# Optimization experiments

Measured on AMD Instinct MI355X. Metric: run time of the kernel, lower is better.

## Reference

```python
import jax, jax.numpy as jnp
import numpy as np

D = 512
H = 8
DH = D // H


def setup_inputs() -> dict:
    key = jax.random.key(0)
    ks = jax.random.split(key, 6)
    B, S = 2, 4096
    scale = 1.0 / np.sqrt(D)
    x = jax.random.normal(ks[0], (B, S, D), dtype=jnp.float32)
    W_q = jax.random.normal(ks[1], (D, D), dtype=jnp.float32) * scale
    W_k = jax.random.normal(ks[2], (D, D), dtype=jnp.float32) * scale
    W_v = jax.random.normal(ks[3], (D, D), dtype=jnp.float32) * scale
    W_proj = jax.random.normal(ks[4], (D, D), dtype=jnp.float32) * scale
    b_proj = jax.random.normal(ks[5], (D,), dtype=jnp.float32) * 0.01
    return {"x": x, "W_q": W_q, "W_k": W_k, "W_v": W_v,
            "W_proj": W_proj, "b_proj": b_proj}


def reference(x, W_q, W_k, W_v, W_proj, b_proj):
    B, S, _ = x.shape
    # torch Linear: y = x @ W.T
    def proj(W):
        y = jnp.einsum('bsd,ed->bse', x, W)
        return y.reshape(B, S, H, DH).transpose(0, 2, 1, 3)  # [B,H,S,DH]
    q, k, v = proj(W_q), proj(W_k), proj(W_v)
    scores = jnp.einsum('bhqd,bhkd->bhqk', q, k) / np.sqrt(DH)  # [B,H,S,S]
    causal = jnp.tril(jnp.ones((S, S), dtype=bool))
    neg = jnp.finfo(scores.dtype).min
    scores = jnp.where(causal[None, None, :, :], scores, neg)
    w = jax.nn.softmax(scores, axis=-1)
    attn = jnp.einsum('bhqk,bhkd->bhqd', w, v)  # [B,H,S,DH]
    attn = attn.transpose(0, 2, 1, 3).reshape(B, S, D)
    return jnp.einsum('bsd,ed->bse', attn, W_proj) + b_proj
```

## Files before the change

kernel.cpp:

```cpp
#include <hip/hip_runtime.h>
#include <hip/hip_bf16.h>
#include <stdint.h>

#define D_MODEL 512
#define NH 8
#define DH 64
#define SEQ 4096
#define NBH 16

typedef __attribute__((ext_vector_type(8))) short bf16x8;
typedef __attribute__((ext_vector_type(4))) float f32x4;
typedef __attribute__((ext_vector_type(16))) float f32x16;

#define CSCALE 0.18033688011112042f

__device__ __forceinline__ uint32_t pkbf(float a, float b) {
    union { float f; uint32_t u; } x, y; x.f = a; y.f = b;
    return __builtin_amdgcn_perm(y.u + 0x8000u, x.u + 0x8000u, 0x07060302u);
}

#define SWZ(R) (((R) + ((R) >> 2)) & 3)

__device__ __forceinline__ bf16x8 cvt8(float4 u, float4 v, float s) {
    union { uint32_t w[4]; bf16x8 h; } r;
    r.w[0] = pkbf(u.x * s, u.y * s); r.w[1] = pkbf(u.z * s, u.w * s);
    r.w[2] = pkbf(v.x * s, v.y * s); r.w[3] = pkbf(v.z * s, v.w * s);
    return r.h;
}

__global__ __launch_bounds__(256) void qkv_kernel(
    const float* __restrict__ x,
    const float* __restrict__ Wq, const float* __restrict__ Wk,
    const float* __restrict__ Wv,
    short* __restrict__ Qb, short* __restrict__ Kb, short* __restrict__ Vt)
{
    __shared__ __align__(16) short at[2][4096];
    __shared__ __align__(16) short bt[2][4096];

    const int tid  = threadIdx.x;
    const int wave = tid >> 6;
    const int lane = tid & 63;
    const int ln = lane & 15, quad = lane >> 4;
    const int z = blockIdx.z;
    const float* W = (z == 0) ? Wq : (z == 1) ? Wk : Wv;
    const float wscale = (z == 0) ? CSCALE : 1.0f;
    const int m0 = blockIdx.x * 128;
    const int n0 = blockIdx.y * 128;
    const int mh = (wave & 1) * 64, nh = (wave >> 1) * 64;

    const int ck0 = tid, ck1 = tid + 256;
    const int R0 = ck0 >> 2, R1 = ck1 >> 2;
    const int c0 = (ck0 & 3) ^ SWZ(R0), c1 = (ck1 & 3) ^ SWZ(R1);

    float4 ra[4], rb[4];
    auto loadAB = [&](int kc) {
        const float* pa0 = x + (size_t)(m0 + R0) * D_MODEL + kc + c0 * 8;
        const float* pa1 = x + (size_t)(m0 + R1) * D_MODEL + kc + c1 * 8;
        ra[0] = *(const float4*)pa0; ra[1] = *(const float4*)(pa0 + 4);
        ra[2] = *(const float4*)pa1; ra[3] = *(const float4*)(pa1 + 4);
        const float* pb0 = W + (size_t)(n0 + R0) * D_MODEL + kc + c0 * 8;
        const float* pb1 = W + (size_t)(n0 + R1) * D_MODEL + kc + c1 * 8;
        rb[0] = *(const float4*)pb0; rb[1] = *(const float4*)(pb0 + 4);
        rb[2] = *(const float4*)pb1; rb[3] = *(const float4*)(pb1 + 4);
    };
    auto writeAB = [&](int buf) {
        *(bf16x8*)&at[buf][ck0 * 8] = cvt8(ra[0], ra[1], 1.0f);
        *(bf16x8*)&at[buf][ck1 * 8] = cvt8(ra[2], ra[3], 1.0f);
        *(bf16x8*)&bt[buf][ck0 * 8] = cvt8(rb[0], rb[1], wscale);
        *(bf16x8*)&bt[buf][ck1 * 8] = cvt8(rb[2], rb[3], wscale);
    };

    f32x4 acc[4][4] = {};

    loadAB(0);
    writeAB(0);

    for (int s = 0; s < 16; ++s) {
        const int cur = s & 1;
        __syncthreads();
        if (s < 15) loadAB((s + 1) * 32);

        bf16x8 a[4], b[4];
#pragma unroll
        for (int i = 0; i < 4; ++i) {
            const int R = mh + i * 16 + ln;
            a[i] = *(const bf16x8*)(&at[cur][R * 32 + ((quad ^ SWZ(R)) * 8)]);
        }
#pragma unroll
        for (int j = 0; j < 4; ++j) {
            const int R = nh + j * 16 + ln;
            b[j] = *(const bf16x8*)(&bt[cur][R * 32 + ((quad ^ SWZ(R)) * 8)]);
        }
#pragma unroll
        for (int i = 0; i < 4; ++i)
#pragma unroll
            for (int j = 0; j < 4; ++j)
                acc[i][j] = __builtin_amdgcn_mfma_f32_16x16x32_bf16(
                    a[i], b[j], acc[i][j], 0, 0, 0);

        if (s < 15) writeAB(cur ^ 1);
    }

    if (z == 2) {
#pragma unroll
        for (int i = 0; i < 4; ++i) {
            const int row0 = m0 + mh + i * 16 + quad * 4;
            const int bb = row0 >> 12, sq = row0 & (SEQ - 1);
#pragma unroll
            for (int j = 0; j < 4; ++j) {
                const int n = n0 + nh + j * 16 + ln;
                const int h = n >> 6, dh = n & 63;
                uint2 st;
                st.x = pkbf(acc[i][j][0], acc[i][j][1]);
                st.y = pkbf(acc[i][j][2], acc[i][j][3]);
                *(uint2*)(Vt + (size_t)((bb * NH + h) * DH + dh) * SEQ + sq) = st;
            }
        }
    } else {
        short* P = (z == 0) ? Qb : Kb;
#pragma unroll
        for (int i = 0; i < 4; ++i)
#pragma unroll
            for (int j = 0; j < 4; ++j) {
                const int n = n0 + nh + j * 16 + ln;
                const int h = n >> 6, dh = n & 63;
                const uint32_t lo = pkbf(acc[i][j][0], acc[i][j][1]);
                const uint32_t hi2 = pkbf(acc[i][j][2], acc[i][j][3]);
#pragma unroll
                for (int r = 0; r < 4; ++r) {
                    const int row = m0 + mh + i * 16 + quad * 4 + r;
                    const int bb = row >> 12, sq = row & (SEQ - 1);
                    const uint32_t w = (r < 2) ? lo : hi2;
                    P[((size_t)((bb * NH + h) * SEQ + sq) << 6) + dh] =
                        (short)((r & 1) ? (w >> 16) : (w & 0xffff));
                }
            }
    }
}

__global__ __launch_bounds__(256) void attn_kernel(
    const short* __restrict__ Qb, const short* __restrict__ Kb,
    const short* __restrict__ Vt, short* __restrict__ ao)
{
    __shared__ __align__(16) short kt[2][4096];
    __shared__ __align__(16) short vt[2][4096];

    const int tid  = threadIdx.x;
    const int wave = tid >> 6;
    const int lane = tid & 63;
    const int l31 = lane & 31, hi = lane >> 5;
    const int bh = blockIdx.y;
    const int w_ = (blockIdx.x + 4 * bh) & 31;
    const int g2 = ((bh >> 3) & 1) ? (31 - w_) : w_;
    const short* Qp = Qb + (size_t)bh * SEQ * DH;
    const short* Kp = Kb + (size_t)bh * SEQ * DH;
    const short* Vp = Vt + (size_t)bh * DH * SEQ;
    const int bb = bh >> 3, h = bh & 7;
    const int q0 = g2 * 128 + wave * 32;
    const int myq = q0 + l31;
    const int jdiag = q0 >> 6;
    const int jmax = 2 * g2 + 1;

    const int ckA = tid, ckB = tid + 256;
    const int RA = ckA >> 3, RB = ckB >> 3;
    const int cA = (ckA & 7) ^ (RA & 7), cB = (ckB & 7) ^ (RB & 7);
    const int RA31 = RA & 31, RB31 = RB & 31;
    const int kkA = (RA & 32) + ((RA31 & 8) << 1) + ((RA31 & 4) << 1)
                  + ((RA31 & 16) >> 2) + (RA31 & 3);
    const int kkB = (RB & 32) + ((RB31 & 8) << 1) + ((RB31 & 4) << 1)
                  + ((RB31 & 16) >> 2) + (RB31 & 3);
    const size_t kOffA = ((size_t)kkA << 6) + cA * 8;
    const size_t kOffB = ((size_t)kkB << 6) + cB * 8;
    const size_t vOffA = (size_t)RA * SEQ + cA * 8;
    const size_t vOffB = (size_t)RB * SEQ + cB * 8;

    bf16x8 sk0, sk1, sv0, sv1;
    auto load_tile = [&](int j) {
        const size_t k0 = (size_t)j * 64;
        sk0 = *(const bf16x8*)(Kp + (k0 << 6) + kOffA);
        sk1 = *(const bf16x8*)(Kp + (k0 << 6) + kOffB);
        sv0 = *(const bf16x8*)(Vp + vOffA + k0);
        sv1 = *(const bf16x8*)(Vp + vOffB + k0);
    };
    auto write_tile = [&](int buf) {
        *(bf16x8*)&kt[buf][ckA * 8] = sk0;
        *(bf16x8*)&kt[buf][ckB * 8] = sk1;
        *(bf16x8*)&vt[buf][ckA * 8] = sv0;
        *(bf16x8*)&vt[buf][ckB * 8] = sv1;
    };

    bf16x8 qf[4];
#pragma unroll
    for (int c = 0; c < 4; ++c)
        qf[c] = *(const bf16x8*)(Qp + (size_t)myq * DH + c * 16 + hi * 8);

    float l_i = 0.f;
    f32x16 o0 = {}, o1 = {};

    load_tile(0);
    write_tile(0);
    load_tile(1);
    __syncthreads();

    for (int j = 0; j <= jmax; ++j) {
        const int cur = j & 1;
        if (j < jmax) {
            write_tile(cur ^ 1);
            if (j + 1 < jmax) load_tile(j + 2);
        }

        f32x16 s0 = {}, s1 = {};
        const int sw = l31 & 7;
#pragma unroll
        for (int c = 0; c < 4; ++c) {
            const int pc = ((2 * c + hi) ^ sw) * 8;
            bf16x8 a0 = *(const bf16x8*)(&kt[cur][l31 * 64 + pc]);
            bf16x8 a1 = *(const bf16x8*)(&kt[cur][(32 + l31) * 64 + pc]);
            s0 = __builtin_amdgcn_mfma_f32_32x32x16_bf16(a0, qf[c], s0, 0, 0, 0);
            s1 = __builtin_amdgcn_mfma_f32_32x32x16_bf16(a1, qf[c], s1, 0, 0, 0);
        }
        if (j >= jdiag) {
            const int k0 = j * 64;
#pragma unroll
            for (int reg = 0; reg < 16; ++reg) {
                const int kl = ((reg >> 2) & 1) * 16 + hi * 8
                             + ((reg >> 3) & 1) * 4 + (reg & 3);
                if (k0 + kl > myq)      s0[reg] = -3e38f;
                if (k0 + 32 + kl > myq) s1[reg] = -3e38f;
            }
        }
#pragma unroll
        for (int i = 0; i < 16; ++i) {
            s0[i] = exp2f(s0[i]);
            s1[i] = exp2f(s1[i]);
        }
        float tr[16];
#pragma unroll
        for (int i = 0; i < 16; ++i) tr[i] = s0[i] + s1[i];
#pragma unroll
        for (int st = 8; st >= 1; st >>= 1)
#pragma unroll
            for (int i = 0; i < st; ++i) tr[i] += tr[i + st];
        l_i += tr[0];

        union { uint32_t u[4]; bf16x8 v; } p00, p01, p10, p11;
        p00.u[0] = pkbf(s0[0], s0[1]);   p00.u[1] = pkbf(s0[2], s0[3]);
        p00.u[2] = pkbf(s0[8], s0[9]);   p00.u[3] = pkbf(s0[10], s0[11]);
        p01.u[0] = pkbf(s0[4], s0[5]);   p01.u[1] = pkbf(s0[6], s0[7]);
        p01.u[2] = pkbf(s0[12], s0[13]); p01.u[3] = pkbf(s0[14], s0[15]);
        p10.u[0] = pkbf(s1[0], s1[1]);   p10.u[1] = pkbf(s1[2], s1[3]);
        p10.u[2] = pkbf(s1[8], s1[9]);   p10.u[3] = pkbf(s1[10], s1[11]);
        p11.u[0] = pkbf(s1[4], s1[5]);   p11.u[1] = pkbf(s1[6], s1[7]);
        p11.u[2] = pkbf(s1[12], s1[13]); p11.u[3] = pkbf(s1[14], s1[15]);

        {
            const short* vrow = &vt[cur][l31 * 64];
            bf16x8 v00 = *(const bf16x8*)(vrow + (((0 + hi) ^ sw) * 8));
            bf16x8 v01 = *(const bf16x8*)(vrow + (((2 + hi) ^ sw) * 8));
            bf16x8 v10 = *(const bf16x8*)(vrow + (((4 + hi) ^ sw) * 8));
            bf16x8 v11 = *(const bf16x8*)(vrow + (((6 + hi) ^ sw) * 8));
            o0 = __builtin_amdgcn_mfma_f32_32x32x16_bf16(v00, p00.v, o0, 0, 0, 0);
            o0 = __builtin_amdgcn_mfma_f32_32x32x16_bf16(v01, p01.v, o0, 0, 0, 0);
            o0 = __builtin_amdgcn_mfma_f32_32x32x16_bf16(v10, p10.v, o0, 0, 0, 0);
            o0 = __builtin_amdgcn_mfma_f32_32x32x16_bf16(v11, p11.v, o0, 0, 0, 0);
        }
        {
            const short* vrow = &vt[cur][(32 + l31) * 64];
            bf16x8 v00 = *(const bf16x8*)(vrow + (((0 + hi) ^ sw) * 8));
            bf16x8 v01 = *(const bf16x8*)(vrow + (((2 + hi) ^ sw) * 8));
            bf16x8 v10 = *(const bf16x8*)(vrow + (((4 + hi) ^ sw) * 8));
            bf16x8 v11 = *(const bf16x8*)(vrow + (((6 + hi) ^ sw) * 8));
            o1 = __builtin_amdgcn_mfma_f32_32x32x16_bf16(v00, p00.v, o1, 0, 0, 0);
            o1 = __builtin_amdgcn_mfma_f32_32x32x16_bf16(v01, p01.v, o1, 0, 0, 0);
            o1 = __builtin_amdgcn_mfma_f32_32x32x16_bf16(v10, p10.v, o1, 0, 0, 0);
            o1 = __builtin_amdgcn_mfma_f32_32x32x16_bf16(v11, p11.v, o1, 0, 0, 0);
        }
        __syncthreads();
    }
    const float l_all = l_i + __shfl_xor(l_i, 32);
    const float inv = 1.0f / l_all;
    short* orow = ao + (size_t)(bb * SEQ + myq) * D_MODEL + h * DH;
#pragma unroll
    for (int c = 0; c < 4; ++c) {
        uint2 st;
        st.x = pkbf(o0[4 * c] * inv,     o0[4 * c + 1] * inv);
        st.y = pkbf(o0[4 * c + 2] * inv, o0[4 * c + 3] * inv);
        *(uint2*)(orow + 8 * c + 4 * hi) = st;
    }
#pragma unroll
    for (int c = 0; c < 4; ++c) {
        uint2 st;
        st.x = pkbf(o1[4 * c] * inv,     o1[4 * c + 1] * inv);
        st.y = pkbf(o1[4 * c + 2] * inv, o1[4 * c + 3] * inv);
        *(uint2*)(orow + 32 + 8 * c + 4 * hi) = st;
    }
}

__global__ __launch_bounds__(256) void proj_kernel(
    const short* __restrict__ attn, const float* __restrict__ Wp,
    const float* __restrict__ bias, float* __restrict__ out)
{
    __shared__ __align__(16) short at[2][2048];
    __shared__ __align__(16) short bt[2][4096];

    const int tid  = threadIdx.x;
    const int wave = tid >> 6;
    const int lane = tid & 63;
    const int ln = lane & 15, quad = lane >> 4;
    const int m0 = blockIdx.x * 64;
    const int n0 = blockIdx.y * 128;
    const int mh = (wave & 1) * 32, nh = (wave >> 1) * 64;

    const int RA = tid >> 2, cAc = (tid & 3) ^ SWZ(RA);
    const int ck0 = tid, ck1 = tid + 256;
    const int R0 = ck0 >> 2, R1 = ck1 >> 2;
    const int c0 = (ck0 & 3) ^ SWZ(R0), c1 = (ck1 & 3) ^ SWZ(R1);

    bf16x8 raA;
    float4 rb[4];
    auto loadAB = [&](int kc) {
        raA = *(const bf16x8*)(attn + (size_t)(m0 + RA) * D_MODEL + kc + cAc * 8);
        const float* pb0 = Wp + (size_t)(n0 + R0) * D_MODEL + kc + c0 * 8;
        const float* pb1 = Wp + (size_t)(n0 + R1) * D_MODEL + kc + c1 * 8;
        rb[0] = *(const float4*)pb0; rb[1] = *(const float4*)(pb0 + 4);
        rb[2] = *(const float4*)pb1; rb[3] = *(const float4*)(pb1 + 4);
    };
    auto writeAB = [&](int buf) {
        *(bf16x8*)&at[buf][tid * 8] = raA;
        *(bf16x8*)&bt[buf][ck0 * 8] = cvt8(rb[0], rb[1], 1.0f);
        *(bf16x8*)&bt[buf][ck1 * 8] = cvt8(rb[2], rb[3], 1.0f);
    };

    f32x4 acc[2][4] = {};

    loadAB(0);
    writeAB(0);

    for (int s = 0; s < 16; ++s) {
        const int cur = s & 1;
        __syncthreads();
        if (s < 15) loadAB((s + 1) * 32);

        bf16x8 a[2], b[4];
#pragma unroll
        for (int i = 0; i < 2; ++i) {
            const int R = mh + i * 16 + ln;
            a[i] = *(const bf16x8*)(&at[cur][R * 32 + ((quad ^ SWZ(R)) * 8)]);
        }
#pragma unroll
        for (int j = 0; j < 4; ++j) {
            const int R = nh + j * 16 + ln;
            b[j] = *(const bf16x8*)(&bt[cur][R * 32 + ((quad ^ SWZ(R)) * 8)]);
        }
#pragma unroll
        for (int i = 0; i < 2; ++i)
#pragma unroll
            for (int j = 0; j < 4; ++j)
                acc[i][j] = __builtin_amdgcn_mfma_f32_16x16x32_bf16(
                    a[i], b[j], acc[i][j], 0, 0, 0);

        if (s < 15) writeAB(cur ^ 1);
    }
#pragma unroll
    for (int j = 0; j < 4; ++j) {
        const int n = n0 + nh + j * 16 + ln;
        const float bv = bias[n];
#pragma unroll
        for (int i = 0; i < 2; ++i)
#pragma unroll
            for (int r = 0; r < 4; ++r) {
                const int row = m0 + mh + i * 16 + quad * 4 + r;
                out[(size_t)row * D_MODEL + n] = acc[i][j][r] + bv;
            }
    }
}

extern "C" void kernel_launch(void* const* d_in, const int* in_sizes, int n_in,
                              void* d_out, int out_size, void* d_ws, size_t ws_size,
                              hipStream_t stream) {
    const float* x  = (const float*)d_in[0];
    const float* Wq = (const float*)d_in[1];
    const float* Wk = (const float*)d_in[2];
    const float* Wv = (const float*)d_in[3];
    const float* Wp = (const float*)d_in[4];
    const float* bp = (const float*)d_in[5];
    float* out = (float*)d_out;

    short* Qb = (short*)d_ws;
    short* Kb = Qb + (size_t)NBH * SEQ * DH;
    short* Vt = Kb + (size_t)NBH * SEQ * DH;
    short* ab = Vt + (size_t)NBH * SEQ * DH;

    qkv_kernel<<<dim3(64, 4, 3), 256, 0, stream>>>(x, Wq, Wk, Wv, Qb, Kb, Vt);
    attn_kernel<<<dim3(32, NBH), 256, 0, stream>>>(Qb, Kb, Vt, ab);
    proj_kernel<<<dim3(128, 4), 256, 0, stream>>>(ab, Wp, bp, out);
}
```

Measured before the change: 201.2 us.

## Stage two KV tiles per barrier and compute row sums via MFMA with ones

Each pipeline stage now loads and processes two 64-key tiles (128 keys), which halves the number of __syncthreads and loop iterations and doubles the shared-memory buffers. The softmax denominator is no longer summed with scalar adds and a cross-lane shuffle. It is accumulated by MFMAs against a ones matrix, using the same bf16-rounded probabilities as the PV product. This frees VALU work, but shared memory grows to 64KB, which may lower occupancy, and four extra MFMAs are added per tile.

```diff
diff --git a/kernel.cpp b/kernel.cpp
--- a/kernel.cpp
+++ b/kernel.cpp
@@ -142,8 +142,8 @@
     const short* __restrict__ Qb, const short* __restrict__ Kb,
     const short* __restrict__ Vt, short* __restrict__ ao)
 {
-    __shared__ __align__(16) short kt[2][4096];
-    __shared__ __align__(16) short vt[2][4096];
+    __shared__ __align__(16) short kt[2][8192];
+    __shared__ __align__(16) short vt[2][8192];
 
     const int tid  = threadIdx.x;
     const int wave = tid >> 6;
@@ -159,7 +159,6 @@
     const int q0 = g2 * 128 + wave * 32;
     const int myq = q0 + l31;
     const int jdiag = q0 >> 6;
-    const int jmax = 2 * g2 + 1;
 
     const int ckA = tid, ckB = tid + 256;
     const int RA = ckA >> 3, RB = ckB >> 3;
@@ -174,19 +173,25 @@
     const size_t vOffA = (size_t)RA * SEQ + cA * 8;
     const size_t vOffB = (size_t)RB * SEQ + cB * 8;
 
-    bf16x8 sk0, sk1, sv0, sv1;
-    auto load_tile = [&](int j) {
-        const size_t k0 = (size_t)j * 64;
-        sk0 = *(const bf16x8*)(Kp + (k0 << 6) + kOffA);
-        sk1 = *(const bf16x8*)(Kp + (k0 << 6) + kOffB);
-        sv0 = *(const bf16x8*)(Vp + vOffA + k0);
-        sv1 = *(const bf16x8*)(Vp + vOffB + k0);
-    };
-    auto write_tile = [&](int buf) {
-        *(bf16x8*)&kt[buf][ckA * 8] = sk0;
-        *(bf16x8*)&kt[buf][ckB * 8] = sk1;
-        *(bf16x8*)&vt[buf][ckA * 8] = sv0;
-        *(bf16x8*)&vt[buf][ckB * 8] = sv1;
+    bf16x8 sk[2][2], sv[2][2];
+    auto load_stage = [&](int s) {
+#pragma unroll
+        for (int sub = 0; sub < 2; ++sub) {
+            const size_t k0 = (size_t)(s * 128 + sub * 64);
+            sk[sub][0] = *(const bf16x8*)(Kp + (k0 << 6) + kOffA);
+            sk[sub][1] = *(const bf16x8*)(Kp + (k0 << 6) + kOffB);
+            sv[sub][0] = *(const bf16x8*)(Vp + vOffA + k0);
+            sv[sub][1] = *(const bf16x8*)(Vp + vOffB + k0);
+        }
+    };
+    auto write_stage = [&](int buf) {
+#pragma unroll
+        for (int sub = 0; sub < 2; ++sub) {
+            *(bf16x8*)&kt[buf][sub * 4096 + ckA * 8] = sk[sub][0];
+            *(bf16x8*)&kt[buf][sub * 4096 + ckB * 8] = sk[sub][1];
+            *(bf16x8*)&vt[buf][sub * 4096 + ckA * 8] = sv[sub][0];
+            *(bf16x8*)&vt[buf][sub * 4096 + ckB * 8] = sv[sub][1];
+        }
     };
 
     bf16x8 qf[4];
@@ -194,91 +199,96 @@
     for (int c = 0; c < 4; ++c)
         qf[c] = *(const bf16x8*)(Qp + (size_t)myq * DH + c * 16 + hi * 8);
 
-    float l_i = 0.f;
-    f32x16 o0 = {}, o1 = {};
-
-    load_tile(0);
-    write_tile(0);
-    load_tile(1);
+    union { uint32_t u[4]; bf16x8 v; } ones;
+#pragma unroll
+    for (int i = 0; i < 4; ++i) ones.u[i] = 0x3F803F80u;
+
+    f32x16 o0 = {}, o1 = {}, lacc = {};
+    const int sw = l31 & 7;
+
+    load_stage(0);
+    write_stage(0);
+    if (g2 > 0) load_stage(1);
     __syncthreads();
 
-    for (int j = 0; j <= jmax; ++j) {
-        const int cur = j & 1;
-        if (j < jmax) {
-            write_tile(cur ^ 1);
-            if (j + 1 < jmax) load_tile(j + 2);
-        }
-
-        f32x16 s0 = {}, s1 = {};
-        const int sw = l31 & 7;
-#pragma unroll
-        for (int c = 0; c < 4; ++c) {
-            const int pc = ((2 * c + hi) ^ sw) * 8;
-            bf16x8 a0 = *(const bf16x8*)(&kt[cur][l31 * 64 + pc]);
-            bf16x8 a1 = *(const bf16x8*)(&kt[cur][(32 + l31) * 64 + pc]);
-            s0 = __builtin_amdgcn_mfma_f32_32x32x16_bf16(a0, qf[c], s0, 0, 0, 0);
-            s1 = __builtin_amdgcn_mfma_f32_32x32x16_bf16(a1, qf[c], s1, 0, 0, 0);
-        }
-        if (j >= jdiag) {
-            const int k0 = j * 64;
-#pragma unroll
-            for (int reg = 0; reg < 16; ++reg) {
-                const int kl = ((reg >> 2) & 1) * 16 + hi * 8
-                             + ((reg >> 3) & 1) * 4 + (reg & 3);
-                if (k0 + kl > myq)      s0[reg] = -3e38f;
-                if (k0 + 32 + kl > myq) s1[reg] = -3e38f;
-            }
-        }
-#pragma unroll
-        for (int i = 0; i < 16; ++i) {
-            s0[i] = exp2f(s0[i]);
-            s1[i] = exp2f(s1[i]);
-        }
-        float tr[16];
-#pragma unroll
-        for (int i = 0; i < 16; ++i) tr[i] = s0[i] + s1[i];
-#pragma unroll
-        for (int st = 8; st >= 1; st >>= 1)
-#pragma unroll
-            for (int i = 0; i < st; ++i) tr[i] += tr[i + st];
-        l_i += tr[0];
-
-        union { uint32_t u[4]; bf16x8 v; } p00, p01, p10, p11;
-        p00.u[0] = pkbf(s0[0], s0[1]);   p00.u[1] = pkbf(s0[2], s0[3]);
-        p00.u[2] = pkbf(s0[8], s0[9]);   p00.u[3] = pkbf(s0[10], s0[11]);
-        p01.u[0] = pkbf(s0[4], s0[5]);   p01.u[1] = pkbf(s0[6], s0[7]);
-        p01.u[2] = pkbf(s0[12], s0[13]); p01.u[3] = pkbf(s0[14], s0[15]);
-        p10.u[0] = pkbf(s1[0], s1[1]);   p10.u[1] = pkbf(s1[2], s1[3]);
-        p10.u[2] = pkbf(s1[8], s1[9]);   p10.u[3] = pkbf(s1[10], s1[11]);
-        p11.u[0] = pkbf(s1[4], s1[5]);   p11.u[1] = pkbf(s1[6], s1[7]);
-        p11.u[2] = pkbf(s1[12], s1[13]); p11.u[3] = pkbf(s1[14], s1[15]);
-
-        {
-            const short* vrow = &vt[cur][l31 * 64];
-            bf16x8 v00 = *(const bf16x8*)(vrow + (((0 + hi) ^ sw) * 8));
-            bf16x8 v01 = *(const bf16x8*)(vrow + (((2 + hi) ^ sw) * 8));
-            bf16x8 v10 = *(const bf16x8*)(vrow + (((4 + hi) ^ sw) * 8));
-            bf16x8 v11 = *(const bf16x8*)(vrow + (((6 + hi) ^ sw) * 8));
-            o0 = __builtin_amdgcn_mfma_f32_32x32x16_bf16(v00, p00.v, o0, 0, 0, 0);
-            o0 = __builtin_amdgcn_mfma_f32_32x32x16_bf16(v01, p01.v, o0, 0, 0, 0);
-            o0 = __builtin_amdgcn_mfma_f32_32x32x16_bf16(v10, p10.v, o0, 0, 0, 0);
-            o0 = __builtin_amdgcn_mfma_f32_32x32x16_bf16(v11, p11.v, o0, 0, 0, 0);
-        }
-        {
-            const short* vrow = &vt[cur][(32 + l31) * 64];
-            bf16x8 v00 = *(const bf16x8*)(vrow + (((0 + hi) ^ sw) * 8));
-            bf16x8 v01 = *(const bf16x8*)(vrow + (((2 + hi) ^ sw) * 8));
-            bf16x8 v10 = *(const bf16x8*)(vrow + (((4 + hi) ^ sw) * 8));
-            bf16x8 v11 = *(const bf16x8*)(vrow + (((6 + hi) ^ sw) * 8));
-            o1 = __builtin_amdgcn_mfma_f32_32x32x16_bf16(v00, p00.v, o1, 0, 0, 0);
-            o1 = __builtin_amdgcn_mfma_f32_32x32x16_bf16(v01, p01.v, o1, 0, 0, 0);
-            o1 = __builtin_amdgcn_mfma_f32_32x32x16_bf16(v10, p10.v, o1, 0, 0, 0);
-            o1 = __builtin_amdgcn_mfma_f32_32x32x16_bf16(v11, p11.v, o1, 0, 0, 0);
+    for (int s = 0; s <= g2; ++s) {
+        const int cur = s & 1;
+        if (s < g2) {
+            write_stage(cur ^ 1);
+            if (s + 1 < g2) load_stage(s + 2);
+        }
+
+#pragma unroll
+        for (int sub = 0; sub < 2; ++sub) {
+            const int j = 2 * s + sub;
+            const short* ktp = &kt[cur][sub * 4096];
+            const short* vtp = &vt[cur][sub * 4096];
+
+            f32x16 s0 = {}, s1 = {};
+#pragma unroll
+            for (int c = 0; c < 4; ++c) {
+                const int pc = ((2 * c + hi) ^ sw) * 8;
+                bf16x8 a0 = *(const bf16x8*)(ktp + l31 * 64 + pc);
+                bf16x8 a1 = *(const bf16x8*)(ktp + (32 + l31) * 64 + pc);
+                s0 = __builtin_amdgcn_mfma_f32_32x32x16_bf16(a0, qf[c], s0, 0, 0, 0);
+                s1 = __builtin_amdgcn_mfma_f32_32x32x16_bf16(a1, qf[c], s1, 0, 0, 0);
+            }
+            if (j >= jdiag) {
+                const int k0 = j * 64;
+#pragma unroll
+                for (int reg = 0; reg < 16; ++reg) {
+                    const int kl = ((reg >> 2) & 1) * 16 + hi * 8
+                                 + ((reg >> 3) & 1) * 4 + (reg & 3);
+                    if (k0 + kl > myq)      s0[reg] = -3e38f;
+                    if (k0 + 32 + kl > myq) s1[reg] = -3e38f;
+                }
+            }
+#pragma unroll
+            for (int i = 0; i < 16; ++i) {
+                s0[i] = exp2f(s0[i]);
+                s1[i] = exp2f(s1[i]);
+            }
+            union { uint32_t u[4]; bf16x8 v; } p00, p01, p10, p11;
+            p00.u[0] = pkbf(s0[0], s0[1]);   p00.u[1] = pkbf(s0[2], s0[3]);
+            p00.u[2] = pkbf(s0[8], s0[9]);   p00.u[3] = pkbf(s0[10], s0[11]);
+            p01.u[0] = pkbf(s0[4], s0[5]);   p01.u[1] = pkbf(s0[6], s0[7]);
+            p01.u[2] = pkbf(s0[12], s0[13]); p01.u[3] = pkbf(s0[14], s0[15]);
+            p10.u[0] = pkbf(s1[0], s1[1]);   p10.u[1] = pkbf(s1[2], s1[3]);
+            p10.u[2] = pkbf(s1[8], s1[9]);   p10.u[3] = pkbf(s1[10], s1[11]);
+            p11.u[0] = pkbf(s1[4], s1[5]);   p11.u[1] = pkbf(s1[6], s1[7]);
+            p11.u[2] = pkbf(s1[12], s1[13]); p11.u[3] = pkbf(s1[14], s1[15]);
+
+            lacc = __builtin_amdgcn_mfma_f32_32x32x16_bf16(ones.v, p00.v, lacc, 0, 0, 0);
+            lacc = __builtin_amdgcn_mfma_f32_32x32x16_bf16(ones.v, p01.v, lacc, 0, 0, 0);
+            lacc = __builtin_amdgcn_mfma_f32_32x32x16_bf16(ones.v, p10.v, lacc, 0, 0, 0);
+            lacc = __builtin_amdgcn_mfma_f32_32x32x16_bf16(ones.v, p11.v, lacc, 0, 0, 0);
+
+            {
+                const short* vrow = vtp + l31 * 64;
+                bf16x8 v00 = *(const bf16x8*)(vrow + (((0 + hi) ^ sw) * 8));
+                bf16x8 v01 = *(const bf16x8*)(vrow + (((2 + hi) ^ sw) * 8));
+                bf16x8 v10 = *(const bf16x8*)(vrow + (((4 + hi) ^ sw) * 8));
+                bf16x8 v11 = *(const bf16x8*)(vrow + (((6 + hi) ^ sw) * 8));
+                o0 = __builtin_amdgcn_mfma_f32_32x32x16_bf16(v00, p00.v, o0, 0, 0, 0);
+                o0 = __builtin_amdgcn_mfma_f32_32x32x16_bf16(v01, p01.v, o0, 0, 0, 0);
+                o0 = __builtin_amdgcn_mfma_f32_32x32x16_bf16(v10, p10.v, o0, 0, 0, 0);
+                o0 = __builtin_amdgcn_mfma_f32_32x32x16_bf16(v11, p11.v, o0, 0, 0, 0);
+            }
+            {
+                const short* vrow = vtp + (32 + l31) * 64;
+                bf16x8 v00 = *(const bf16x8*)(vrow + (((0 + hi) ^ sw) * 8));
+                bf16x8 v01 = *(const bf16x8*)(vrow + (((2 + hi) ^ sw) * 8));
+                bf16x8 v10 = *(const bf16x8*)(vrow + (((4 + hi) ^ sw) * 8));
+                bf16x8 v11 = *(const bf16x8*)(vrow + (((6 + hi) ^ sw) * 8));
+                o1 = __builtin_amdgcn_mfma_f32_32x32x16_bf16(v00, p00.v, o1, 0, 0, 0);
+                o1 = __builtin_amdgcn_mfma_f32_32x32x16_bf16(v01, p01.v, o1, 0, 0, 0);
+                o1 = __builtin_amdgcn_mfma_f32_32x32x16_bf16(v10, p10.v, o1, 0, 0, 0);
+                o1 = __builtin_amdgcn_mfma_f32_32x32x16_bf16(v11, p11.v, o1, 0, 0, 0);
+            }
         }
         __syncthreads();
     }
-    const float l_all = l_i + __shfl_xor(l_i, 32);
-    const float inv = 1.0f / l_all;
+    const float inv = 1.0f / lacc[0];
     short* orow = ao + (size_t)(bb * SEQ + myq) * D_MODEL + h * DH;
 #pragma unroll
     for (int c = 0; c < 4; ++c) {
```

Result: slower. 207.2 us (+3.0%).
